# Optimization experiments

Measured on AMD Instinct MI355X. Metric: run time of the kernel, lower is better.

## Reference

```python
import jax, jax.numpy as jnp
import numpy as np

B, C, H, W = 16, 256, 56, 56
HEADS = 4
C_OUT = 256
K = 3
SQ = 16  # squeeze_rate (C=256 >= 80, so not halved)
BN_EPS = 1e-5


def setup_inputs() -> dict:
    key = jax.random.key(0)
    ks = jax.random.split(key, 9)
    r = C // SQ
    cper = C_OUT // HEADS
    return {
        "x": jax.random.normal(ks[0], (B, C, H, W), dtype=jnp.float32),
        "bn_gamma": 1.0 + 0.1 * jax.random.normal(ks[1], (C,), dtype=jnp.float32),
        "bn_beta": 0.1 * jax.random.normal(ks[2], (C,), dtype=jnp.float32),
        "bn_mean": 0.1 * jax.random.normal(ks[3], (C,), dtype=jnp.float32),
        "bn_var": 0.5 + jax.random.uniform(ks[4], (C,), dtype=jnp.float32),
        "fc1_w": 0.1 * jax.random.normal(ks[5], (HEADS, r, C), dtype=jnp.float32),
        "fc2_w": 0.1 * jax.random.normal(ks[6], (HEADS, C, r), dtype=jnp.float32),
        "fc2_b": jnp.ones((HEADS, C), dtype=jnp.float32),  # init.constant_(bias, 1.0)
        "conv_w": 0.05 * jax.random.normal(ks[7], (HEADS, cper, C, K, K), dtype=jnp.float32),
        "inactive_channels": 192,
    }


def reference(x, bn_gamma, bn_beta, bn_mean, bn_var, fc1_w, fc2_w, fc2_b, conv_w, inactive_channels):
    b, c, h, w = x.shape
    heads = fc1_w.shape[0]
    # BatchNorm (inference, running stats) + ReLU
    inv = jax.lax.rsqrt(bn_var + BN_EPS)
    xn = jax.nn.relu((x - bn_mean[None, :, None, None]) * (bn_gamma * inv)[None, :, None, None]
                     + bn_beta[None, :, None, None])
    # Global average pool -> [b, c]
    x_avg = xn.mean(axis=(2, 3))
    # Per-head SE gate: relu(fc2(relu(fc1(x_avg))))  -> [heads, b, c]
    y1 = jax.nn.relu(jnp.einsum("bc,hrc->hbr", x_avg, fc1_w))
    mask = jax.nn.relu(jnp.einsum("hbr,hcr->hbc", y1, fc2_w) + fc2_b[:, None, :])
    lasso_loss = mask.mean(axis=(1, 2)).sum()  # sum over heads of per-head mean
    # topk smallest -> threshold; zero out mask values <= k-th smallest (detached cmp)
    mask_d = jax.lax.stop_gradient(mask)
    if inactive_channels > 0:
        neg_vals, _ = jax.lax.top_k(-mask_d, inactive_channels)  # k largest of -mask
        thresh = -neg_vals[..., -1:]  # k-th smallest of mask, [heads, b, 1]
        mask_c = jnp.where(mask_d <= thresh, 0.0, mask)
    else:
        mask_c = mask
    # Apply per-head channel mask and stack heads: [b, heads*c, h, w]
    mc = jnp.transpose(mask_c, (1, 0, 2))  # [b, heads, c]
    x_mask = (xn[:, None, :, :, :] * mc[:, :, :, None, None]).reshape(b, heads * c, h, w)
    # Grouped conv (groups=heads), weight [heads*cper, c, K, K]
    wflat = conv_w.reshape(-1, c, K, K)
    out = jax.lax.conv_general_dilated(
        x_mask, wflat, window_strides=(1, 1), padding=[(1, 1), (1, 1)],
        dimension_numbers=("NCHW", "OIHW", "NCHW"), feature_group_count=heads)
    bo, co, ho, wo = out.shape
    out = out.reshape(bo, heads, co // heads, ho, wo).transpose(0, 2, 1, 3, 4).reshape(bo, co, ho, wo)
    return out, lasso_loss
```

## Files before the change

kernel.cpp:

```cpp
#include <hip/hip_runtime.h>
#include <hip/hip_bf16.h>
#include <math.h>

#define B_     16
#define C_     256
#define H_     56
#define W_     56
#define HEADS_ 4
#define CPER_  64
#define R_     16
#define HW_    (H_*W_)
#define BN_EPS_ 1e-5f

typedef short bf16x8 __attribute__((ext_vector_type(8)));
typedef float f32x4  __attribute__((ext_vector_type(4)));

__device__ inline unsigned short f2bf(float f) {
    unsigned int u = __builtin_bit_cast(unsigned int, f);
    u += 0x7fffu + ((u >> 16) & 1u);
    return (unsigned short)(u >> 16);
}

__global__ __launch_bounds__(64) void k_pool(
    const float* __restrict__ x,
    const float* __restrict__ gamma, const float* __restrict__ beta,
    const float* __restrict__ mean,  const float* __restrict__ var,
    float* __restrict__ xavg)
{
    int plane = blockIdx.x;
    int c = plane & (C_ - 1);
    float s = gamma[c] * rsqrtf(var[c] + BN_EPS_);
    float t = fmaf(-mean[c], s, beta[c]);
    const float4* xp = (const float4*)(x + (size_t)plane * HW_);
    float sum = 0.f;
    for (int i = threadIdx.x; i < HW_ / 4; i += 64) {
        float4 v = xp[i];
        sum += fmaxf(fmaf(v.x, s, t), 0.f) + fmaxf(fmaf(v.y, s, t), 0.f)
             + fmaxf(fmaf(v.z, s, t), 0.f) + fmaxf(fmaf(v.w, s, t), 0.f);
    }
    for (int off = 32; off; off >>= 1) sum += __shfl_down(sum, off, 64);
    if (threadIdx.x == 0) xavg[plane] = sum * (1.f / HW_);
}

__global__ __launch_bounds__(256) void k_wt2(const float* __restrict__ w,
                                             float* __restrict__ wt2f)
{
    int i = blockIdx.x * 256 + threadIdx.x;
    if (i >= HEADS_ * 9 * CPER_ * C_) return;
    int c = i & 255, j = (i >> 8) & 63, ht = i >> 14;
    int h = ht / 9, t = ht - h * 9;
    wt2f[i] = w[((size_t)((h * CPER_ + j) * C_ + c)) * 9 + t];
}

__global__ __launch_bounds__(256) void k_se(
    const float* __restrict__ xavg,
    const float* __restrict__ fc1, const float* __restrict__ fc2,
    const float* __restrict__ fc2b, const int* __restrict__ kptr,
    float* __restrict__ maskc, int* __restrict__ aidx64,
    int* __restrict__ act_cnt, float* __restrict__ lasso)
{
    int hb = blockIdx.x;
    int h = hb / B_, b = hb - h * B_;
    int tid = threadIdx.x;

    __shared__ float sav[C_], sy1[R_], smask[C_], sred[4], sthr;
    __shared__ int scnt, s_ord[C_];

    sav[tid] = xavg[b * C_ + tid];
    if (tid == 0) scnt = 0;
    __syncthreads();

    if (tid < R_) {
        const float* w = fc1 + (size_t)(h * R_ + tid) * C_;
        float acc = 0.f;
        for (int c2 = 0; c2 < C_; ++c2) acc = fmaf(sav[c2], w[c2], acc);
        sy1[tid] = fmaxf(acc, 0.f);
    }
    __syncthreads();

    const float* w2 = fc2 + (size_t)(h * C_ + tid) * R_;
    float acc = fc2b[h * C_ + tid];
    for (int r = 0; r < R_; ++r) acc = fmaf(sy1[r], w2[r], acc);
    float m = fmaxf(acc, 0.f);
    smask[tid] = m;
    __syncthreads();

    float ls = m;
    for (int off = 32; off > 0; off >>= 1) ls += __shfl_down(ls, off, 64);
    int lane = tid & 63, wv = tid >> 6;
    if (lane == 0) sred[wv] = ls;

    int cl = 0, ce = 0;
    for (int j = 0; j < C_; ++j) {
        float vj = smask[j];
        cl += (vj < m);
        ce += (vj == m);
    }
    if (tid == 0) sthr = -1e30f;
    __syncthreads();
    int k = kptr[0];
    if (k > 0 && cl <= k - 1 && (k - 1) < cl + ce) sthr = m;
    __syncthreads();

    float thr = sthr;
    float mc = (m <= thr) ? 0.f : m;
    maskc[hb * C_ + tid] = mc;
    if (mc != 0.f) {
        int p = atomicAdd(&scnt, 1);
        s_ord[p] = tid;
    }
    __syncthreads();
    if (tid < 64) aidx64[hb * 64 + tid] = (tid < scnt) ? s_ord[tid] : 0;
    if (tid == 0) {
        act_cnt[hb] = scnt;
        atomicAdd(lasso, (sred[0] + sred[1] + sred[2] + sred[3]) * (1.f / (B_ * C_)));
    }
}

__global__ __launch_bounds__(256) void k_wgather(
    const float* __restrict__ wt2f, const float* __restrict__ maskc,
    const int* __restrict__ aidx64, const int* __restrict__ acnt,
    short* __restrict__ Wc)
{
    int t = blockIdx.x, hb = blockIdx.y;
    int h = hb >> 4;
    int tid = threadIdx.x;
    int cnt = acnt[hb];
    __shared__ int s_act[64];
    __shared__ float s_mv[64];
    if (tid < 64) {
        int a = aidx64[hb * 64 + tid];
        s_act[tid] = a;
        s_mv[tid]  = (tid < cnt) ? maskc[hb * C_ + a] : 0.f;
    }
    __syncthreads();
    const float* wsrc = wt2f + (size_t)(h * 9 + t) * (CPER_ * C_);
    short* wdst = Wc + (size_t)(hb * 9 + t) * (CPER_ * 64);
    for (int it = 0; it < 16; ++it) {
        int e = it * 256 + tid;
        int cp = e & 63, j = e >> 6;
        float v = wsrc[j * C_ + s_act[cp]] * s_mv[cp];
        wdst[e] = (short)f2bf(v);
    }
}

__global__ __launch_bounds__(256) void k_bnc(
    const float* __restrict__ x,
    const float* __restrict__ gamma, const float* __restrict__ beta,
    const float* __restrict__ mean,  const float* __restrict__ var,
    const int* __restrict__ aidx64, short* __restrict__ xc)
{
    int y = blockIdx.x, b = blockIdx.y;
    int tid = threadIdx.x;
    __shared__ unsigned short T[W_ * 258];
    __shared__ float ss[C_], st[C_];
    __shared__ short sact[256];

    {
        float s = gamma[tid] * rsqrtf(var[tid] + BN_EPS_);
        ss[tid] = s;
        st[tid] = fmaf(-mean[tid], s, beta[tid]);
        int h = tid >> 6, cp = tid & 63;
        sact[tid] = (short)aidx64[(h * B_ + b) * 64 + cp];
    }
    __syncthreads();

    const float* xrow = x + (size_t)b * C_ * HW_ + y * W_;
    for (int i = tid; i < C_ * 14; i += 256) {
        int c = i / 14, f = i - c * 14;
        float4 v = *(const float4*)(xrow + (size_t)c * HW_ + f * 4);
        float s = ss[c], t = st[c];
        int xb = f * 4;
        T[(xb + 0) * 258 + c] = f2bf(fmaxf(fmaf(v.x, s, t), 0.f));
        T[(xb + 1) * 258 + c] = f2bf(fmaxf(fmaf(v.y, s, t), 0.f));
        T[(xb + 2) * 258 + c] = f2bf(fmaxf(fmaf(v.z, s, t), 0.f));
        T[(xb + 3) * 258 + c] = f2bf(fmaxf(fmaf(v.w, s, t), 0.f));
    }
    __syncthreads();

    unsigned int* ob = (unsigned int*)xc;
    #pragma unroll
    for (int h = 0; h < HEADS_; ++h) {
        size_t obase = ((size_t)(h * B_ + b) * HW_ + (size_t)y * W_) * 32;
        for (int i = tid; i < W_ * 32; i += 256) {
            int px = i >> 5, d = i & 31;
            unsigned int lo = T[px * 258 + sact[h * 64 + 2 * d]];
            unsigned int hi = T[px * 258 + sact[h * 64 + 2 * d + 1]];
            ob[obase + i] = lo | (hi << 16);
        }
    }
}

__global__ __launch_bounds__(256, 3) void k_conv(
    const short* __restrict__ xc, const short* __restrict__ Wc,
    const int* __restrict__ acnt, float* __restrict__ out)
{
    int g = blockIdx.x;
    int vx = g & 7, r = g >> 3;
    int hb = vx * 8 + r / 14;
    int band = r - (r / 14) * 14;
    int h = hb >> 4, b = hb & 15;
    int tid = threadIdx.x, lane = tid & 63, w = tid >> 6;
    int y0 = band * 4;
    int cnt = acnt[hb];
    int cntp = (cnt + 31) & ~31;

    __shared__ short sX[6 * 66 * 64];

    {
        const short* xb = xc + (size_t)hb * HW_ * 64;
        for (int row = 0; row < 6; ++row) {
            int gy = y0 + row - 1;
            bool yok = (gy >= 0 && gy < H_);
            for (int e = tid; e < 66 * 8; e += 256) {
                int col = e >> 3, ck = e & 7;
                int gx = col - 1;
                bf16x8 v = {0, 0, 0, 0, 0, 0, 0, 0};
                if (yok && gx >= 0 && gx < W_)
                    v = *(const bf16x8*)(xb + ((size_t)(gy * W_ + gx)) * 64 + ck * 8);
                int slot = ((ck << 3) + ((col & 7) << 3)) & 63;
                *(bf16x8*)(sX + (row * 66 + col) * 64 + slot) = v;
            }
        }
    }
    __syncthreads();

    f32x4 acc[4][4];
    #pragma unroll
    for (int i = 0; i < 4; ++i)
        #pragma unroll
        for (int j = 0; j < 4; ++j)
            #pragma unroll
            for (int rr = 0; rr < 4; ++rr) acc[i][j][rr] = 0.f;

    int m = lane & 15, q = lane >> 4;
    const unsigned int* sXu = (const unsigned int*)sX;
    const short* Wh = Wc + (size_t)hb * 9 * 4096;
    int yrow = y0 + w;

    for (int t = 0; t < 9; ++t) {
        int dy = t / 3 - 1, dx = t - (t / 3) * 3 - 1;
        int srow = w + dy + 1;
        int coln = m + dx + 1;
        int sb8 = (coln & 7) << 3;
        const short* Wt = Wh + t * 4096 + m * 64 + q * 8;
        int ub = (srow * 66 + coln) * 32;
        for (int c0 = 0; c0 < cntp; c0 += 32) {
            bf16x8 aF[4], bF[4];
            #pragma unroll
            for (int jt = 0; jt < 4; ++jt)
                aF[jt] = *(const bf16x8*)(Wt + jt * 1024 + c0);
            int slot = (c0 + q * 8 + sb8) & 63;
            #pragma unroll
            for (int xt = 0; xt < 4; ++xt)
                bF[xt] = *(const bf16x8*)&sXu[ub + xt * 512 + (slot >> 1)];
            #pragma unroll
            for (int jt = 0; jt < 4; ++jt)
                #pragma unroll
                for (int xt = 0; xt < 4; ++xt)
                    acc[jt][xt] = __builtin_amdgcn_mfma_f32_16x16x32_bf16(
                        aF[jt], bF[xt], acc[jt][xt], 0, 0, 0);
        }
    }

    #pragma unroll
    for (int xt = 0; xt < 4; ++xt) {
        int xx = xt * 16 + m;
        if (xx < W_) {
            #pragma unroll
            for (int jt = 0; jt < 4; ++jt)
                #pragma unroll
                for (int rr = 0; rr < 4; ++rr) {
                    int j = jt * 16 + q * 4 + rr;
                    int oc = j * HEADS_ + h;
                    out[(((size_t)b * C_ + oc) * H_ + yrow) * W_ + xx] = acc[jt][xt][rr];
                }
        }
    }
}

extern "C" void kernel_launch(void* const* d_in, const int* in_sizes, int n_in,
                              void* d_out, int out_size, void* d_ws, size_t ws_size,
                              hipStream_t stream)
{
    const float* x     = (const float*)d_in[0];
    const float* gamma = (const float*)d_in[1];
    const float* beta  = (const float*)d_in[2];
    const float* mean  = (const float*)d_in[3];
    const float* var   = (const float*)d_in[4];
    const float* fc1   = (const float*)d_in[5];
    const float* fc2   = (const float*)d_in[6];
    const float* fc2b  = (const float*)d_in[7];
    const float* convw = (const float*)d_in[8];
    const int*   kptr  = (const int*)d_in[9];

    float* out   = (float*)d_out;
    float* lasso = out + (size_t)B_ * C_ * HW_;

    char* ws = (char*)d_ws;
    size_t off = 0;
    short* xc    = (short*)(ws + off); off += (size_t)HEADS_ * B_ * HW_ * 64 * 2;
    off = (off + 255) & ~(size_t)255;
    float* xavg  = (float*)(ws + off); off += (size_t)B_ * C_ * 4;
    float* maskc = (float*)(ws + off); off += (size_t)HEADS_ * B_ * C_ * 4;
    int*   aidx64= (int*)  (ws + off); off += (size_t)HEADS_ * B_ * 64 * 4;
    int*   acnt  = (int*)  (ws + off); off += (size_t)HEADS_ * B_ * 4;
    off = (off + 255) & ~(size_t)255;
    float* wt2f  = (float*)(ws + off); off += (size_t)HEADS_ * 9 * CPER_ * C_ * 4;
    off = (off + 255) & ~(size_t)255;
    short* Wc    = (short*)(ws + off); off += (size_t)HEADS_ * B_ * 9 * CPER_ * 64 * 2;

    hipMemsetAsync(lasso, 0, 4, stream);

    k_wt2<<<(HEADS_ * 9 * CPER_ * C_ + 255) / 256, 256, 0, stream>>>(convw, wt2f);
    k_pool<<<B_ * C_, 64, 0, stream>>>(x, gamma, beta, mean, var, xavg);
    k_se<<<HEADS_ * B_, 256, 0, stream>>>(xavg, fc1, fc2, fc2b, kptr,
                                          maskc, aidx64, acnt, lasso);
    k_wgather<<<dim3(9, HEADS_ * B_), 256, 0, stream>>>(wt2f, maskc, aidx64, acnt, Wc);
    k_bnc<<<dim3(H_, B_), 256, 0, stream>>>(x, gamma, beta, mean, var, aidx64, xc);
    k_conv<<<HEADS_ * B_ * (H_ / 4), 256, 0, stream>>>(xc, Wc, acnt, out);
}
```

Baseline: 202.8 us.

## Stage weights in double-buffered LDS and read activations directly from global

```diff
diff --git a/kernel.cpp b/kernel.cpp
--- a/kernel.cpp
+++ b/kernel.cpp
@@ -140,7 +140,8 @@
         int e = it * 256 + tid;
         int cp = e & 63, j = e >> 6;
         float v = wsrc[j * C_ + s_act[cp]] * s_mv[cp];
-        wdst[e] = (short)f2bf(v);
+        int slot = (cp + 8 * (j & 7)) & 63;
+        wdst[j * 64 + slot] = (short)f2bf(v);
     }
 }
 
@@ -193,35 +194,28 @@
 
 __global__ __launch_bounds__(256, 3) void k_conv(
     const short* __restrict__ xc, const short* __restrict__ Wc,
-    const int* __restrict__ acnt, float* __restrict__ out)
+    float* __restrict__ out)
 {
     int g = blockIdx.x;
     int vx = g & 7, r = g >> 3;
     int hb = vx * 8 + r / 14;
     int band = r - (r / 14) * 14;
     int h = hb >> 4, b = hb & 15;
-    int tid = threadIdx.x, lane = tid & 63, w = tid >> 6;
+    int tid = threadIdx.x, lane = tid & 63, wv = tid >> 6;
     int y0 = band * 4;
-    int cnt = acnt[hb];
-    int cntp = (cnt + 31) & ~31;
-
-    __shared__ short sX[6 * 66 * 64];
+    int m = lane & 15, q = lane >> 4;
+
+    __shared__ short sW[2][4096];
+
+    const short* Wh = Wc + (size_t)hb * 9 * 4096;
+    const short* xb = xc + (size_t)hb * HW_ * 64;
+    int soff = wv * 512 + lane * 8;
 
     {
-        const short* xb = xc + (size_t)hb * HW_ * 64;
-        for (int row = 0; row < 6; ++row) {
-            int gy = y0 + row - 1;
-            bool yok = (gy >= 0 && gy < H_);
-            for (int e = tid; e < 66 * 8; e += 256) {
-                int col = e >> 3, ck = e & 7;
-                int gx = col - 1;
-                bf16x8 v = {0, 0, 0, 0, 0, 0, 0, 0};
-                if (yok && gx >= 0 && gx < W_)
-                    v = *(const bf16x8*)(xb + ((size_t)(gy * W_ + gx)) * 64 + ck * 8);
-                int slot = ((ck << 3) + ((col & 7) << 3)) & 63;
-                *(bf16x8*)(sX + (row * 66 + col) * 64 + slot) = v;
-            }
-        }
+        bf16x8 w0 = *(const bf16x8*)(Wh + soff);
+        bf16x8 w1 = *(const bf16x8*)(Wh + 2048 + soff);
+        *(bf16x8*)&sW[0][soff] = w0;
+        *(bf16x8*)&sW[0][2048 + soff] = w1;
     }
     __syncthreads();
 
@@ -233,27 +227,36 @@
             #pragma unroll
             for (int rr = 0; rr < 4; ++rr) acc[i][j][rr] = 0.f;
 
-    int m = lane & 15, q = lane >> 4;
-    const unsigned int* sXu = (const unsigned int*)sX;
-    const short* Wh = Wc + (size_t)hb * 9 * 4096;
-    int yrow = y0 + w;
-
+    int yrow = y0 + wv;
+    int arot = q * 8 + 8 * (m & 7);
+
+    #pragma unroll
     for (int t = 0; t < 9; ++t) {
-        int dy = t / 3 - 1, dx = t - (t / 3) * 3 - 1;
-        int srow = w + dy + 1;
-        int coln = m + dx + 1;
-        int sb8 = (coln & 7) << 3;
-        const short* Wt = Wh + t * 4096 + m * 64 + q * 8;
-        int ub = (srow * 66 + coln) * 32;
-        for (int c0 = 0; c0 < cntp; c0 += 32) {
+        const int dy = t / 3 - 1, dx = t % 3 - 1;
+        bf16x8 w0, w1;
+        if (t < 8) {
+            const short* Wn = Wh + (t + 1) * 4096;
+            w0 = *(const bf16x8*)(Wn + soff);
+            w1 = *(const bf16x8*)(Wn + 2048 + soff);
+        }
+        int gy = yrow + dy;
+        bool gyok = (unsigned)gy < (unsigned)H_;
+        const short* sWc = sW[t & 1];
+
+        #pragma unroll
+        for (int c0 = 0; c0 < 64; c0 += 32) {
             bf16x8 aF[4], bF[4];
             #pragma unroll
             for (int jt = 0; jt < 4; ++jt)
-                aF[jt] = *(const bf16x8*)(Wt + jt * 1024 + c0);
-            int slot = (c0 + q * 8 + sb8) & 63;
-            #pragma unroll
-            for (int xt = 0; xt < 4; ++xt)
-                bF[xt] = *(const bf16x8*)&sXu[ub + xt * 512 + (slot >> 1)];
+                aF[jt] = *(const bf16x8*)&sWc[(jt * 16 + m) * 64 + ((c0 + arot) & 63)];
+            #pragma unroll
+            for (int xt = 0; xt < 4; ++xt) {
+                int gx = xt * 16 + m + dx;
+                bf16x8 v = {0, 0, 0, 0, 0, 0, 0, 0};
+                if (gyok && (unsigned)gx < (unsigned)W_)
+                    v = *(const bf16x8*)(xb + ((size_t)(gy * W_ + gx)) * 64 + c0 + q * 8);
+                bF[xt] = v;
+            }
             #pragma unroll
             for (int jt = 0; jt < 4; ++jt)
                 #pragma unroll
@@ -261,6 +264,11 @@
                     acc[jt][xt] = __builtin_amdgcn_mfma_f32_16x16x32_bf16(
                         aF[jt], bF[xt], acc[jt][xt], 0, 0, 0);
         }
+        if (t < 8) {
+            *(bf16x8*)&sW[(t + 1) & 1][soff] = w0;
+            *(bf16x8*)&sW[(t + 1) & 1][2048 + soff] = w1;
+        }
+        __syncthreads();
     }
 
     #pragma unroll
@@ -318,5 +326,5 @@
                                           maskc, aidx64, acnt, lasso);
     k_wgather<<<dim3(9, HEADS_ * B_), 256, 0, stream>>>(wt2f, maskc, aidx64, acnt, Wc);
     k_bnc<<<dim3(H_, B_), 256, 0, stream>>>(x, gamma, beta, mean, var, aidx64, xc);
-    k_conv<<<HEADS_ * B_ * (H_ / 4), 256, 0, stream>>>(xc, Wc, acnt, out);
-}
+    k_conv<<<HEADS_ * B_ * (H_ / 4), 256, 0, stream>>>(xc, Wc, out);
+}
```

Measured after the change: 194.3 us. -4.2%, faster.
